# Kernel tuning notes

Measured on AMD Instinct MI355X. Metric: run time of the kernel, lower is better.

Reference implementation:

```python
import jax, jax.numpy as jnp
import numpy as np

SIGMA = 45.0
N, M, D = 4096, 4096, 1024


def setup_inputs() -> dict:
    key = jax.random.key(0)
    k1, k2 = jax.random.split(key)
    inputs = jax.random.normal(k1, (N, D), dtype=jnp.float32)
    samples = jax.random.normal(k2, (M, D), dtype=jnp.float32)
    return {"inputs": inputs, "samples": samples}


def _sq_dists(x, y):
    # ||x_i||^2 + ||y_j||^2 - 2 x_i.y_j  -> [N, M]
    prod = x @ y.T
    xs = jnp.sum(x * x, axis=1)[:, None]
    ys = jnp.sum(y * y, axis=1)[None, :]
    return xs + ys - 2.0 * prod


def reference(inputs, samples):
    n = inputs.shape[0]
    m = samples.shape[0]
    x = inputs.reshape(n, -1)
    y = samples.reshape(m, -1)
    inv_s2 = 1.0 / (SIGMA ** 2)

    k_xx = _sq_dists(x, x)
    k_yy = _sq_dists(y, y)
    k_xy = _sq_dists(x, y)

    # unbiased MMD: exclude diagonal terms of k_xx, k_yy
    exx = jnp.exp(-k_xx * inv_s2)
    eyy = jnp.exp(-k_yy * inv_s2)
    exy = jnp.exp(-k_xy * inv_s2)

    mmd = (jnp.sum(exx) - jnp.sum(jnp.exp(-jnp.diag(k_xx) * inv_s2))) / (n * (n - 1))
    mmd = mmd + (jnp.sum(eyy) - jnp.sum(jnp.exp(-jnp.diag(k_yy) * inv_s2))) / (m * (m - 1))
    mmd = mmd - 2.0 / (n * m) * jnp.sum(exy)
    return mmd
```

## Files before the change

### kernel.cpp

```cpp
#include <hip/hip_runtime.h>
#include <math.h>


typedef _Float16 f16_t;
typedef _Float16 f16x4 __attribute__((ext_vector_type(4)));
typedef _Float16 f16x8 __attribute__((ext_vector_type(8)));
typedef float floatx4 __attribute__((ext_vector_type(4)));

#define NROWS 4096
#define MROWS 4096
#define DDIM  1024
#define BM    256
#define BN    128
#define BK    32
#define NKT   (DDIM / BK)
#define PSTRIDE (4096 * BK)
#define NTR   (NROWS / BM)
#define NTC   (NROWS / BN)
#define XXB   272
#define NBLK  (2 * XXB + NTR * NTC)

__global__ __launch_bounds__(256) void convert_kernel(
    const float* __restrict__ X, const float* __restrict__ Y,
    f16_t* __restrict__ Xp, f16_t* __restrict__ Yp,
    float* __restrict__ nx, float* __restrict__ ny) {
    const int wid  = threadIdx.x >> 6;
    const int lane = threadIdx.x & 63;
    const int row  = blockIdx.x * 4 + wid;
    const float* src;
    f16_t* dstp;
    float* nrm;
    int r;
    if (row < NROWS) {
        r = row;         src = X + (size_t)r * DDIM;
        dstp = Xp;  nrm = nx;
    } else {
        r = row - NROWS; src = Y + (size_t)r * DDIM;
        dstp = Yp;  nrm = ny;
    }
    const float4* s4 = (const float4*)src;
    float s = 0.f;
    #pragma unroll
    for (int c = 0; c < 4; c++) {
        float4 v = s4[c * 64 + lane];
        f16x4 h;
        h[0] = (f16_t)v.x; h[1] = (f16_t)v.y;
        h[2] = (f16_t)v.z; h[3] = (f16_t)v.w;
        *(f16x4*)(dstp + (size_t)(c * 8 + (lane >> 3)) * PSTRIDE
                       + (size_t)r * BK + (lane & 7) * 4) = h;
        float h0 = (float)h[0], h1 = (float)h[1];
        float h2 = (float)h[2], h3 = (float)h[3];
        s += h0 * h0 + h1 * h1 + h2 * h2 + h3 * h3;
    }
    #pragma unroll
    for (int off = 32; off > 0; off >>= 1) s += __shfl_down(s, off);
    if (lane == 0) nrm[r] = s;
}

#define STAGE(tt_) do {                                                        \
    const int slot_ = (tt_) & 3;                                               \
    const size_t kk_ = (size_t)(tt_) * PSTRIDE;                                \
    __builtin_amdgcn_global_load_lds(                                          \
        (const __attribute__((address_space(1))) void*)(gA + kk_),             \
        (__attribute__((address_space(3))) void*)(&ldsA[slot_][wave * 1024]),  \
        16, 0, 0);                                                             \
    __builtin_amdgcn_global_load_lds(                                          \
        (const __attribute__((address_space(1))) void*)(gA + kk_ + 16 * BK),   \
        (__attribute__((address_space(3))) void*)(&ldsA[slot_][wave * 1024 + 512]), \
        16, 0, 0);                                                             \
    __builtin_amdgcn_global_load_lds(                                          \
        (const __attribute__((address_space(1))) void*)(gB + kk_),             \
        (__attribute__((address_space(3))) void*)(&ldsB[slot_][wave * 512]),   \
        16, 0, 0);                                                             \
  } while (0)

#define VMCNT3 asm volatile("s_waitcnt vmcnt(3)" ::: "memory")
#define VMCNT0 asm volatile("s_waitcnt vmcnt(0)" ::: "memory")
#define BAR    __builtin_amdgcn_s_barrier()

#define DSREAD(slot_, AH_, BH_) do {                                           \
    _Pragma("unroll")                                                          \
    for (int s_ = 0; s_ < 4; s_++) {                                           \
        AH_[s_] = *(const f16x8*)&ldsA[slot_][aoff + s_ * 16 * BK];            \
        BH_[s_] = *(const f16x8*)&ldsB[slot_][boff + s_ * 16 * BK];            \
    }                                                                          \
  } while (0)

#define MFMA16(AH_, BH_) do {                                                  \
    __builtin_amdgcn_s_setprio(1);                                             \
    _Pragma("unroll")                                                          \
    for (int i_ = 0; i_ < 4; i_++)                                             \
        _Pragma("unroll")                                                      \
        for (int j_ = 0; j_ < 4; j_++)                                         \
            acc[i_][j_] = __builtin_amdgcn_mfma_f32_16x16x32_f16(              \
                AH_[i_], BH_[j_], acc[i_][j_], 0, 0, 0);                       \
    __builtin_amdgcn_s_setprio(0);                                             \
  } while (0)

__global__ __launch_bounds__(512, 2) void mmd_mfma(
    const f16_t* __restrict__ Xp, const f16_t* __restrict__ Yp,
    const float* __restrict__ nx, const float* __restrict__ ny,
    double* __restrict__ partials) {
    __shared__ __align__(16) f16_t ldsA[4][BM * BK];
    __shared__ __align__(16) f16_t ldsB[4][BN * BK];
    __shared__ double wred[8];

    const int b = blockIdx.x;
    const f16_t *Abase, *Bbase;
    const float *nAp, *nBp;
    int arow0, brow0;
    double coef;
    if (b < 2 * XXB) {
        int u = (b < XXB) ? b : b - XXB;
        int i = 0;
        while (u >= NTC - 2 * i) { u -= NTC - 2 * i; i++; }
        const int ti = i, tj = 2 * i + u;
        const double w = (tj >= 2 * i + 2) ? 2.0 : 1.0;
        const f16_t* base;
        const float* nb_;
        double denom;
        if (b < XXB) { base = Xp; nb_ = nx; denom = (double)NROWS * (double)(NROWS - 1); }
        else         { base = Yp; nb_ = ny; denom = (double)MROWS * (double)(MROWS - 1); }
        Abase = base; Bbase = base;
        arow0 = ti * BM;  brow0 = tj * BN;
        nAp = nb_ + ti * BM;  nBp = nb_ + tj * BN;
        coef = w / denom;
    } else {
        const int u = b - 2 * XXB;
        const int ti = u >> 5, tj = u & 31;
        Abase = Xp; Bbase = Yp;
        arow0 = ti * BM;  brow0 = tj * BN;
        nAp = nx + ti * BM;  nBp = ny + tj * BN;
        coef = -2.0 / ((double)NROWS * (double)MROWS);
    }

    const int tid  = threadIdx.x;
    const int wave = tid >> 6;
    const int lane = tid & 63;
    const int wm   = wave >> 1;
    const int wn   = wave & 1;
    const int m    = lane & 15;
    const int quad = lane >> 4;
    const int sw8  = (quad ^ ((m >> 1) & 3)) * 8;
    const int aoff = (wm * 64 + m) * BK + sw8;
    const int boff = (wn * 64 + m) * BK + sw8;

    const int lr = lane >> 2;
    const int lc = (lane & 3) ^ ((lane >> 3) & 3);
    const f16_t* gA = Abase + (size_t)(arow0 + wave * 32 + lr) * BK + lc * 8;
    const f16_t* gB = Bbase + (size_t)(brow0 + wave * 16 + lr) * BK + lc * 8;

    floatx4 acc[4][4];
    #pragma unroll
    for (int i = 0; i < 4; i++)
        #pragma unroll
        for (int j = 0; j < 4; j++) acc[i][j] = (floatx4){0.f, 0.f, 0.f, 0.f};

    f16x8 ahA[4], bhA[4], ahB[4], bhB[4];

    STAGE(0); STAGE(1);
    VMCNT3;
    BAR;
    DSREAD(0, ahA, bhA);

    for (int tt = 0; tt < NKT - 4; tt += 4) {
        STAGE(tt + 2); VMCNT3; BAR; DSREAD(1, ahB, bhB); MFMA16(ahA, bhA);
        STAGE(tt + 3); VMCNT3; BAR; DSREAD(2, ahA, bhA); MFMA16(ahB, bhB);
        STAGE(tt + 4); VMCNT3; BAR; DSREAD(3, ahB, bhB); MFMA16(ahA, bhA);
        STAGE(tt + 5); VMCNT3; BAR; DSREAD(0, ahA, bhA); MFMA16(ahB, bhB);
    }
    STAGE(30); VMCNT3; BAR; DSREAD(1, ahB, bhB); MFMA16(ahA, bhA);
    STAGE(31); VMCNT3; BAR; DSREAD(2, ahA, bhA); MFMA16(ahB, bhB);
    VMCNT0;              BAR; DSREAD(3, ahB, bhB); MFMA16(ahA, bhA);
    MFMA16(ahB, bhB);

    const float inv_s2 = 1.0f / 2025.0f;
    float nbv[4];
    #pragma unroll
    for (int j = 0; j < 4; j++) nbv[j] = nBp[wn * 64 + j * 16 + m];
    float lsum = 0.f;
    #pragma unroll
    for (int i = 0; i < 4; i++) {
        floatx4 na4 = *(const floatx4*)&nAp[wm * 64 + i * 16 + quad * 4];
        #pragma unroll
        for (int j = 0; j < 4; j++)
            #pragma unroll
            for (int r = 0; r < 4; r++) {
                float arg = (2.f * acc[i][j][r] - na4[r] - nbv[j]) * inv_s2;
                lsum += __expf(arg);
            }
    }

    double d = (double)lsum;
    #pragma unroll
    for (int off = 32; off > 0; off >>= 1) d += __shfl_down(d, off);
    if (lane == 0) wred[wave] = d;
    __syncthreads();
    if (tid == 0) {
        double s = 0.0;
        #pragma unroll
        for (int w = 0; w < 8; w++) s += wred[w];
        partials[b] = s * coef;
    }
}

__global__ __launch_bounds__(256) void final_reduce(const double* __restrict__ partials,
                                                    float* __restrict__ out) {
    __shared__ double red[256];
    int t = threadIdx.x;
    double s = 0.0;
    for (int i = t; i < NBLK; i += 256) s += partials[i];
    red[t] = s;
    __syncthreads();
    for (int off = 128; off > 0; off >>= 1) {
        if (t < off) red[t] += red[t + off];
        __syncthreads();
    }
    if (t == 0) {
        double mmd = red[0] - 1.0 / (double)(NROWS - 1) - 1.0 / (double)(MROWS - 1);
        out[0] = (float)mmd;
    }
}

extern "C" void kernel_launch(void* const* d_in, const int* in_sizes, int n_in,
                              void* d_out, int out_size, void* d_ws, size_t ws_size,
                              hipStream_t stream) {
    const float* X = (const float*)d_in[0];
    const float* Y = (const float*)d_in[1];
    float* out = (float*)d_out;

    char* p = (char*)d_ws;
    double* partials = (double*)p;            p += ((size_t)NBLK * sizeof(double) + 255) & ~255ULL;
    float* nx = (float*)p;                    p += (size_t)NROWS * sizeof(float);
    float* ny = (float*)p;                    p += (size_t)MROWS * sizeof(float);
    f16_t* Xp = (f16_t*)p;                    p += (size_t)NROWS * DDIM * sizeof(f16_t);
    f16_t* Yp = (f16_t*)p;

    convert_kernel<<<(NROWS + MROWS) / 4, 256, 0, stream>>>(X, Y, Xp, Yp, nx, ny);
    mmd_mfma<<<NBLK, 512, 0, stream>>>(Xp, Yp, nx, ny, partials);
    final_reduce<<<1, 256, 0, stream>>>(partials, out);
}
```

Baseline: 166.6 us.

## Restructure GEMM pipeline to three LDS slots, swizzle block order, raise occupancy

```diff
diff --git a/kernel.cpp b/kernel.cpp
--- a/kernel.cpp
+++ b/kernel.cpp
@@ -57,8 +57,7 @@
     if (lane == 0) nrm[r] = s;
 }
 
-#define STAGE(tt_) do {                                                        \
-    const int slot_ = (tt_) & 3;                                               \
+#define STAGE(tt_, slot_) do {                                                 \
     const size_t kk_ = (size_t)(tt_) * PSTRIDE;                                \
     __builtin_amdgcn_global_load_lds(                                          \
         (const __attribute__((address_space(1))) void*)(gA + kk_),             \
@@ -74,7 +73,6 @@
         16, 0, 0);                                                             \
   } while (0)
 
-#define VMCNT3 asm volatile("s_waitcnt vmcnt(3)" ::: "memory")
 #define VMCNT0 asm volatile("s_waitcnt vmcnt(0)" ::: "memory")
 #define BAR    __builtin_amdgcn_s_barrier()
 
@@ -97,15 +95,24 @@
     __builtin_amdgcn_s_setprio(0);                                             \
   } while (0)
 
-__global__ __launch_bounds__(512, 2) void mmd_mfma(
+#define PHASE(st_, ss_, rs_, AHR_, BHR_, AHC_, BHC_) do {                      \
+    BAR;                                                                       \
+    STAGE(st_, ss_);                                                           \
+    DSREAD(rs_, AHR_, BHR_);                                                   \
+    MFMA16(AHC_, BHC_);                                                        \
+    VMCNT0;                                                                    \
+  } while (0)
+
+__global__ __launch_bounds__(512, 4) void mmd_mfma(
     const f16_t* __restrict__ Xp, const f16_t* __restrict__ Yp,
     const float* __restrict__ nx, const float* __restrict__ ny,
     double* __restrict__ partials) {
-    __shared__ __align__(16) f16_t ldsA[4][BM * BK];
-    __shared__ __align__(16) f16_t ldsB[4][BN * BK];
+    __shared__ __align__(16) f16_t ldsA[3][BM * BK];
+    __shared__ __align__(16) f16_t ldsB[3][BN * BK];
     __shared__ double wred[8];
 
-    const int b = blockIdx.x;
+    const int b = ((blockIdx.x & 7) * (NBLK / 8)) + (blockIdx.x >> 3);
+
     const f16_t *Abase, *Bbase;
     const float *nAp, *nBp;
     int arow0, brow0;
@@ -158,20 +165,22 @@
 
     f16x8 ahA[4], bhA[4], ahB[4], bhB[4];
 
-    STAGE(0); STAGE(1);
-    VMCNT3;
+    STAGE(0, 0); STAGE(1, 1);
+    VMCNT0;
     BAR;
     DSREAD(0, ahA, bhA);
 
-    for (int tt = 0; tt < NKT - 4; tt += 4) {
-        STAGE(tt + 2); VMCNT3; BAR; DSREAD(1, ahB, bhB); MFMA16(ahA, bhA);
-        STAGE(tt + 3); VMCNT3; BAR; DSREAD(2, ahA, bhA); MFMA16(ahB, bhB);
-        STAGE(tt + 4); VMCNT3; BAR; DSREAD(3, ahB, bhB); MFMA16(ahA, bhA);
-        STAGE(tt + 5); VMCNT3; BAR; DSREAD(0, ahA, bhA); MFMA16(ahB, bhB);
-    }
-    STAGE(30); VMCNT3; BAR; DSREAD(1, ahB, bhB); MFMA16(ahA, bhA);
-    STAGE(31); VMCNT3; BAR; DSREAD(2, ahA, bhA); MFMA16(ahB, bhB);
-    VMCNT0;              BAR; DSREAD(3, ahB, bhB); MFMA16(ahA, bhA);
+    for (int tt = 0; tt < NKT - 2; tt += 6) {
+        PHASE(tt + 2, 2, 1, ahB, bhB, ahA, bhA);
+        PHASE(tt + 3, 0, 2, ahA, bhA, ahB, bhB);
+        PHASE(tt + 4, 1, 0, ahB, bhB, ahA, bhA);
+        PHASE(tt + 5, 2, 1, ahA, bhA, ahB, bhB);
+        PHASE(tt + 6, 0, 2, ahB, bhB, ahA, bhA);
+        PHASE(tt + 7, 1, 0, ahA, bhA, ahB, bhB);
+    }
+    BAR;
+    DSREAD(1, ahB, bhB);
+    MFMA16(ahA, bhA);
     MFMA16(ahB, bhB);
 
     const float inv_s2 = 1.0f / 2025.0f;
```

After: 326.0 us. 1.96x slower.

## Load B fragments directly to registers and reorder block-to-tile mapping

Applied to the files above, without the earlier changes.

```diff
diff --git a/kernel.cpp b/kernel.cpp
--- a/kernel.cpp
+++ b/kernel.cpp
@@ -57,8 +57,7 @@
     if (lane == 0) nrm[r] = s;
 }
 
-#define STAGE(tt_) do {                                                        \
-    const int slot_ = (tt_) & 3;                                               \
+#define STAGEA(tt_, slot_) do {                                                \
     const size_t kk_ = (size_t)(tt_) * PSTRIDE;                                \
     __builtin_amdgcn_global_load_lds(                                          \
         (const __attribute__((address_space(1))) void*)(gA + kk_),             \
@@ -68,22 +67,24 @@
         (const __attribute__((address_space(1))) void*)(gA + kk_ + 16 * BK),   \
         (__attribute__((address_space(3))) void*)(&ldsA[slot_][wave * 1024 + 512]), \
         16, 0, 0);                                                             \
-    __builtin_amdgcn_global_load_lds(                                          \
-        (const __attribute__((address_space(1))) void*)(gB + kk_),             \
-        (__attribute__((address_space(3))) void*)(&ldsB[slot_][wave * 512]),   \
-        16, 0, 0);                                                             \
-  } while (0)
-
-#define VMCNT3 asm volatile("s_waitcnt vmcnt(3)" ::: "memory")
-#define VMCNT0 asm volatile("s_waitcnt vmcnt(0)" ::: "memory")
-#define BAR    __builtin_amdgcn_s_barrier()
-
-#define DSREAD(slot_, AH_, BH_) do {                                           \
+  } while (0)
+
+#define BLOAD(tt_, BH_) do {                                                   \
+    const size_t kk_ = (size_t)(tt_) * PSTRIDE;                                \
     _Pragma("unroll")                                                          \
-    for (int s_ = 0; s_ < 4; s_++) {                                           \
+    for (int s_ = 0; s_ < 4; s_++)                                             \
+        BH_[s_] = *(const f16x8*)(gBfrag + kk_ + s_ * 16 * BK);                \
+  } while (0)
+
+#define VM6   asm volatile("s_waitcnt vmcnt(6)" ::: "memory")
+#define VM4   asm volatile("s_waitcnt vmcnt(4)" ::: "memory")
+#define VM0   asm volatile("s_waitcnt vmcnt(0)" ::: "memory")
+#define BAR   __builtin_amdgcn_s_barrier()
+
+#define DSREADA(slot_, AH_) do {                                               \
+    _Pragma("unroll")                                                          \
+    for (int s_ = 0; s_ < 4; s_++)                                             \
         AH_[s_] = *(const f16x8*)&ldsA[slot_][aoff + s_ * 16 * BK];            \
-        BH_[s_] = *(const f16x8*)&ldsB[slot_][boff + s_ * 16 * BK];            \
-    }                                                                          \
   } while (0)
 
 #define MFMA16(AH_, BH_) do {                                                  \
@@ -97,15 +98,24 @@
     __builtin_amdgcn_s_setprio(0);                                             \
   } while (0)
 
+#define PH(st_, ss_, rs_, AHR_, BHR_, AHC_, BHC_) do {                         \
+    STAGEA(st_, ss_);                                                          \
+    BLOAD((st_) - 1, BHR_);                                                    \
+    VM6;                                                                       \
+    BAR;                                                                       \
+    DSREADA(rs_, AHR_);                                                        \
+    MFMA16(AHC_, BHC_);                                                        \
+  } while (0)
+
 __global__ __launch_bounds__(512, 2) void mmd_mfma(
     const f16_t* __restrict__ Xp, const f16_t* __restrict__ Yp,
     const float* __restrict__ nx, const float* __restrict__ ny,
     double* __restrict__ partials) {
     __shared__ __align__(16) f16_t ldsA[4][BM * BK];
-    __shared__ __align__(16) f16_t ldsB[4][BN * BK];
     __shared__ double wred[8];
 
-    const int b = blockIdx.x;
+    const int b = ((blockIdx.x & 7) * (NBLK / 8)) + (blockIdx.x >> 3);
+
     const f16_t *Abase, *Bbase;
     const float *nAp, *nBp;
     int arow0, brow0;
@@ -143,12 +153,11 @@
     const int quad = lane >> 4;
     const int sw8  = (quad ^ ((m >> 1) & 3)) * 8;
     const int aoff = (wm * 64 + m) * BK + sw8;
-    const int boff = (wn * 64 + m) * BK + sw8;
 
     const int lr = lane >> 2;
     const int lc = (lane & 3) ^ ((lane >> 3) & 3);
     const f16_t* gA = Abase + (size_t)(arow0 + wave * 32 + lr) * BK + lc * 8;
-    const f16_t* gB = Bbase + (size_t)(brow0 + wave * 16 + lr) * BK + lc * 8;
+    const f16_t* gBfrag = Bbase + (size_t)(brow0 + wn * 64 + m) * BK + quad * 8;
 
     floatx4 acc[4][4];
     #pragma unroll
@@ -156,22 +165,28 @@
         #pragma unroll
         for (int j = 0; j < 4; j++) acc[i][j] = (floatx4){0.f, 0.f, 0.f, 0.f};
 
-    f16x8 ahA[4], bhA[4], ahB[4], bhB[4];
-
-    STAGE(0); STAGE(1);
-    VMCNT3;
+    f16x8 ahA[4], ahB[4], bhA[4], bhB[4];
+
+    STAGEA(0, 0); STAGEA(1, 1);
+    BLOAD(0, bhA);
+    VM6;
     BAR;
-    DSREAD(0, ahA, bhA);
+    DSREADA(0, ahA);
 
     for (int tt = 0; tt < NKT - 4; tt += 4) {
-        STAGE(tt + 2); VMCNT3; BAR; DSREAD(1, ahB, bhB); MFMA16(ahA, bhA);
-        STAGE(tt + 3); VMCNT3; BAR; DSREAD(2, ahA, bhA); MFMA16(ahB, bhB);
-        STAGE(tt + 4); VMCNT3; BAR; DSREAD(3, ahB, bhB); MFMA16(ahA, bhA);
-        STAGE(tt + 5); VMCNT3; BAR; DSREAD(0, ahA, bhA); MFMA16(ahB, bhB);
-    }
-    STAGE(30); VMCNT3; BAR; DSREAD(1, ahB, bhB); MFMA16(ahA, bhA);
-    STAGE(31); VMCNT3; BAR; DSREAD(2, ahA, bhA); MFMA16(ahB, bhB);
-    VMCNT0;              BAR; DSREAD(3, ahB, bhB); MFMA16(ahA, bhA);
+        PH(tt + 2, 2, 1, ahB, bhB, ahA, bhA);
+        PH(tt + 3, 3, 2, ahA, bhA, ahB, bhB);
+        PH(tt + 4, 0, 3, ahB, bhB, ahA, bhA);
+        PH(tt + 5, 1, 0, ahA, bhA, ahB, bhB);
+    }
+    PH(30, 2, 1, ahB, bhB, ahA, bhA);
+    PH(31, 3, 2, ahA, bhA, ahB, bhB);
+    BLOAD(31, bhB);
+    VM4;
+    BAR;
+    DSREADA(3, ahB);
+    MFMA16(ahA, bhA);
+    VM0;
     MFMA16(ahB, bhB);
 
     const float inv_s2 = 1.0f / 2025.0f;
```

Result: slower. 186.1 us (+11.7%).
